# Performance work log

Hardware: AMD Instinct MI355X
Metric: run time of the kernel (lower is better)

The kernel has to match this reference:

```python
import jax, jax.numpy as jnp
import numpy as np

T, B, D, R, H = 16, 1024, 1024, 8, 16
DH = D // H


def setup_inputs() -> dict:
    key = jax.random.key(0)
    ks = jax.random.split(key, 10)
    s = 1.0 / np.sqrt(D)
    return {
        "table_embs": jax.random.normal(ks[0], (T, B, D), jnp.float32),
        "rel_embs": jax.random.normal(ks[1], (T, R, D), jnp.float32),
        "rel_idx": jax.random.randint(ks[2], (T, R), 0, T),
        "Wq": jax.random.normal(ks[3], (D, D), jnp.float32) * s,
        "bq": jnp.zeros((D,), jnp.float32),
        "Wk": jax.random.normal(ks[4], (D, D), jnp.float32) * s,
        "bk": jnp.zeros((D,), jnp.float32),
        "Wv": jax.random.normal(ks[5], (D, D), jnp.float32) * s,
        "bv": jnp.zeros((D,), jnp.float32),
        "Wo": jax.random.normal(ks[6], (D, D), jnp.float32) * s,
        "bo": jnp.zeros((D,), jnp.float32),
        "w_rel": jax.random.normal(ks[7], (D,), jnp.float32) * s,
        "b_rel": jnp.zeros((1,), jnp.float32),
    }


def reference(table_embs, rel_embs, rel_idx, Wq, bq, Wk, bk, Wv, bv, Wo, bo, w_rel, b_rel):
    # relationship weights: sigmoid(Linear(rel_emb)) -> scalar per (table, relation)
    rel_w = jax.nn.sigmoid(rel_embs @ w_rel + b_rel[0])          # [T, R]
    # gather related tables' embeddings and apply relationship weight
    others = table_embs[rel_idx]                                  # [T, R, B, D]
    weighted = others * rel_w[:, :, None, None]                   # [T, R, B, D]
    kv_src = jnp.transpose(weighted, (0, 2, 1, 3))                # [T, B, R, D]
    # MultiheadAttention, q_len=1, kv_len=R (PyTorch convention: x @ W.T + b)
    q = (table_embs @ Wq.T + bq).reshape(T, B, H, DH)             # [T, B, H, DH]
    k = (kv_src @ Wk.T + bk).reshape(T, B, R, H, DH)              # [T, B, R, H, DH]
    v = (kv_src @ Wv.T + bv).reshape(T, B, R, H, DH)
    scores = jnp.einsum("tbhd,tbrhd->tbhr", q, k) / np.sqrt(DH)   # [T, B, H, R]
    attn = jax.nn.softmax(scores, axis=-1)
    ctx = jnp.einsum("tbhr,tbrhd->tbhd", attn, v).reshape(T, B, D)
    return ctx @ Wo.T + bo                                        # [T, B, D]
```

## Files before the change

### kernel.cpp

```cpp
#include <hip/hip_runtime.h>


typedef unsigned short u16;
typedef __attribute__((ext_vector_type(8))) short short8;
typedef __attribute__((ext_vector_type(4))) float f32x4;

__device__ __forceinline__ float bf2f(u16 u) {
  unsigned int x = ((unsigned int)u) << 16;
  return __uint_as_float(x);
}
__device__ __forceinline__ u16 f2bf(float f) {
  unsigned int x = __float_as_uint(f);
  unsigned int r = (x + 0x7fffu + ((x >> 16) & 1u)) >> 16;
  return (u16)r;
}

__device__ __forceinline__ void gld_lds16(const void* g, void* l) {
  __builtin_amdgcn_global_load_lds(
      (const __attribute__((address_space(1))) unsigned int*)(unsigned long long)g,
      (__attribute__((address_space(3))) unsigned int*)(unsigned int)(unsigned long long)l,
      16, 0, 0);
}


__global__ void relw_kernel(const float* __restrict__ rel_embs,
                            const float* __restrict__ w_rel,
                            const float* __restrict__ b_rel,
                            float* __restrict__ rel_w) {
  const int tr = blockIdx.x;
  const float* row = rel_embs + (size_t)tr * 1024;
  const int lane = threadIdx.x;
  float s = 0.f;
  for (int i = lane; i < 1024; i += 64) s += row[i] * w_rel[i];
  for (int off = 32; off > 0; off >>= 1) s += __shfl_down(s, off, 64);
  if (lane == 0) rel_w[tr] = 1.f / (1.f + __expf(-(s + b_rel[0])));
}

__global__ void cvt_f32_bf16(const float* __restrict__ in, u16* __restrict__ out, int n4) {
  int i = blockIdx.x * blockDim.x + threadIdx.x;
  if (i >= n4) return;
  float4 v = ((const float4*)in)[i];
  ushort4 o;
  o.x = f2bf(v.x); o.y = f2bf(v.y); o.z = f2bf(v.z); o.w = f2bf(v.w);
  ((ushort4*)out)[i] = o;
}

__global__ void cvt_w4(const float* __restrict__ Wq, const float* __restrict__ Wk,
                       const float* __restrict__ Wv, const float* __restrict__ Wo,
                       u16* __restrict__ Wcat, u16* __restrict__ Wob) {
  const int i = blockIdx.x * 256 + threadIdx.x;
  const int w = i >> 18;
  const int j = i & 0x3ffff;
  const float* src = (w == 0) ? Wq : (w == 1) ? Wk : (w == 2) ? Wv : Wo;
  u16* dst = (w == 3) ? Wob : (Wcat + ((size_t)w << 20));
  float4 v = ((const float4*)src)[j];
  ushort4 o;
  o.x = f2bf(v.x); o.y = f2bf(v.y); o.z = f2bf(v.z); o.w = f2bf(v.w);
  ((ushort4*)dst)[j] = o;
}


__device__ __forceinline__ void mainloop256(const u16* __restrict__ A,
                                            const u16* __restrict__ B,
                                            u16* lds, int m0, int n0,
                                            f32x4 (&acc)[8][4]) {
  const int tid  = threadIdx.x;
  const int lane = tid & 63;
  const int w    = tid >> 6;
  const int wm   = w >> 2, wn = w & 3;
  const int fr   = lane & 15, fq = lane >> 4;
  const int swz  = fr & 7;

  const unsigned A0 = 0, B0 = 16384, A1 = 32768, B1 = 49152;

  const int srow = tid >> 3;
  const int lc   = (tid & 7) ^ (srow & 7);
  const u16* a0p = A + (size_t)(m0 + srow) * 1024 + lc * 8;
  const u16* b0p = B + (size_t)(n0 + srow) * 1024 + lc * 8;
  const unsigned d0 = (unsigned)((tid & ~63) * 8);

  const u16 *ap0[2], *ap1[2], *bp0[2], *bp1[2];
#pragma unroll
  for (int ks = 0; ks < 2; ++ks) {
    const unsigned ck = (unsigned)((((ks << 2) + fq) ^ swz) << 3);
    ap0[ks] = lds + A0 + (wm * 128 + fr) * 64 + ck;
    ap1[ks] = lds + A1 + (wm * 128 + fr) * 64 + ck;
    bp0[ks] = lds + B0 + (wn * 64 + fr) * 64 + ck;
    bp1[ks] = lds + B1 + (wn * 64 + fr) * 64 + ck;
  }

#define STAGE4(g, AO, BO)                                                      \
  do {                                                                         \
    gld_lds16(a0p + (2*(g))   * 65536, lds + (AO) + d0 + (2*(g))   * 4096);    \
    gld_lds16(a0p + (2*(g)+1) * 65536, lds + (AO) + d0 + (2*(g)+1) * 4096);    \
    gld_lds16(b0p + (2*(g))   * 65536, lds + (BO) + d0 + (2*(g))   * 4096);    \
    gld_lds16(b0p + (2*(g)+1) * 65536, lds + (BO) + d0 + (2*(g)+1) * 4096);    \
  } while (0)

#define PHASE_Q(q, ap, STMT)                                                   \
  do {                                                                         \
    short8 a0k0 = *(const short8*)((ap)[0] + (2*(q))   * 1024);                \
    short8 a1k0 = *(const short8*)((ap)[0] + (2*(q)+1) * 1024);                \
    short8 a0k1 = *(const short8*)((ap)[1] + (2*(q))   * 1024);                \
    short8 a1k1 = *(const short8*)((ap)[1] + (2*(q)+1) * 1024);                \
    STMT;                                                                      \
    __builtin_amdgcn_s_barrier();                                              \
    asm volatile("s_waitcnt lgkmcnt(0)" ::: "memory");                         \
    __builtin_amdgcn_sched_barrier(0);                                         \
    __builtin_amdgcn_s_setprio(1);                                             \
    _Pragma("unroll")                                                          \
    for (int j = 0; j < 4; ++j) {                                              \
      acc[2*(q)][j]   = __builtin_amdgcn_mfma_f32_16x16x32_bf16(a0k0, bgv[j][0], acc[2*(q)][j],   0, 0, 0); \
      acc[2*(q)+1][j] = __builtin_amdgcn_mfma_f32_16x16x32_bf16(a1k0, bgv[j][0], acc[2*(q)+1][j], 0, 0, 0); \
    }                                                                          \
    _Pragma("unroll")                                                          \
    for (int j = 0; j < 4; ++j) {                                              \
      acc[2*(q)][j]   = __builtin_amdgcn_mfma_f32_16x16x32_bf16(a0k1, bgv[j][1], acc[2*(q)][j],   0, 0, 0); \
      acc[2*(q)+1][j] = __builtin_amdgcn_mfma_f32_16x16x32_bf16(a1k1, bgv[j][1], acc[2*(q)+1][j], 0, 0, 0); \
    }                                                                          \
    __builtin_amdgcn_s_setprio(0);                                             \
  } while (0)

#define KTILE(ap, bp, AO_N, BO_N, SG)                                          \
  do {                                                                         \
    short8 bgv[4][2];                                                          \
    _Pragma("unroll")                                                          \
    for (int j = 0; j < 4; ++j) {                                              \
      bgv[j][0] = *(const short8*)((bp)[0] + j * 1024);                        \
      bgv[j][1] = *(const short8*)((bp)[1] + j * 1024);                        \
    }                                                                          \
    PHASE_Q(0, ap, { if (SG) STAGE4(0, AO_N, BO_N); });                        \
    __builtin_amdgcn_s_barrier();                                              \
    PHASE_Q(1, ap, { if (SG) { STAGE4(1, AO_N, BO_N); a0p += 64; b0p += 64; } }); \
    __builtin_amdgcn_s_barrier();                                              \
    PHASE_Q(2, ap, {});                                                        \
    __builtin_amdgcn_s_barrier();                                              \
    PHASE_Q(3, ap, {});                                                        \
    if (SG) asm volatile("s_waitcnt vmcnt(0)" ::: "memory");                   \
    __builtin_amdgcn_s_barrier();                                              \
  } while (0)

#pragma unroll
  for (int r = 0; r < 4; ++r) {
    gld_lds16(a0p + r * 65536, lds + A0 + d0 + r * 4096);
    gld_lds16(b0p + r * 65536, lds + B0 + d0 + r * 4096);
  }
  a0p += 64; b0p += 64;
  asm volatile("s_waitcnt vmcnt(0)" ::: "memory");
  __builtin_amdgcn_s_barrier();

  for (int it = 0; it < 8; ++it) {
    KTILE(ap0, bp0, A1, B1, true);
    KTILE(ap1, bp1, A0, B0, (it < 7));
  }
#undef STAGE4
#undef PHASE_Q
#undef KTILE
}

__global__ __launch_bounds__(512, 2)
void gemm_qkv(const u16* __restrict__ A, const u16* __restrict__ Bw,
              const float* __restrict__ bq,
              u16* __restrict__ Qt, u16* __restrict__ Kt, u16* __restrict__ Vt) {
  __shared__ __align__(16) u16 lds[65536];
  const int n0 = blockIdx.x * 256;
  const int m0 = blockIdx.y * 256;
  f32x4 acc[8][4];
#pragma unroll
  for (int i = 0; i < 8; ++i)
#pragma unroll
    for (int j = 0; j < 4; ++j) acc[i][j] = (f32x4){0.f, 0.f, 0.f, 0.f};

  mainloop256(A, Bw, lds, m0, n0, acc);

  const int tid  = threadIdx.x;
  const int lane = tid & 63;
  const int w    = tid >> 6;
  const int wm   = w >> 2, wn = w & 3;
  const int colw = lane & 15, roww = (lane >> 4) * 4;
  const int t = m0 >> 10, b0 = m0 & 1023;
  const int sel = n0 >> 10, dbase = n0 & 1023;
  u16* outp = (sel == 0) ? Qt : (sel == 1) ? Kt : Vt;

  for (int pass = 0; pass < 2; ++pass) {
    if (wm == pass) {
#pragma unroll
      for (int j = 0; j < 4; ++j) {
        const int dl = wn * 64 + j * 16 + colw;
        const float badd = (sel == 0) ? bq[dbase + dl] : 0.f;
#pragma unroll
        for (int i = 0; i < 8; ++i) {
          const int bl = i * 16 + roww;
          const unsigned p0 = (unsigned)f2bf(acc[i][j][0] + badd)
                            | ((unsigned)f2bf(acc[i][j][1] + badd) << 16);
          const unsigned p1 = (unsigned)f2bf(acc[i][j][2] + badd)
                            | ((unsigned)f2bf(acc[i][j][3] + badd) << 16);
          *(unsigned*)(lds + dl * 136 + bl)     = p0;
          *(unsigned*)(lds + dl * 136 + bl + 2) = p1;
        }
      }
    }
    __syncthreads();
#pragma unroll
    for (int rr = 0; rr < 8; ++rr) {
      const int slot = rr * 512 + tid;
      const int row = slot >> 4, c16 = slot & 15;
      const uint4 v = *(const uint4*)(lds + row * 136 + c16 * 8);
      *(uint4*)(outp + ((size_t)t << 20) + (size_t)(dbase + row) * 1024
                + b0 + pass * 128 + c16 * 8) = v;
    }
    __syncthreads();
  }
}

__global__ __launch_bounds__(512, 2)
void gemm_out(const u16* __restrict__ A, const u16* __restrict__ Bw,
              const float* __restrict__ bo, float* __restrict__ out) {
  __shared__ __align__(16) u16 lds[65536];
  const int n0 = blockIdx.x * 256;
  const int m0 = blockIdx.y * 256;
  f32x4 acc[8][4];
#pragma unroll
  for (int i = 0; i < 8; ++i)
#pragma unroll
    for (int j = 0; j < 4; ++j) acc[i][j] = (f32x4){0.f, 0.f, 0.f, 0.f};

  mainloop256(A, Bw, lds, m0, n0, acc);

  const int lane = threadIdx.x & 63;
  const int w    = threadIdx.x >> 6;
  const int wm   = w >> 2, wn = w & 3;
  const int colw = lane & 15, roww = (lane >> 4) * 4;
#pragma unroll
  for (int j = 0; j < 4; ++j) {
    const int gn = n0 + wn * 64 + j * 16 + colw;
    const float bov = bo[gn];
#pragma unroll
    for (int i = 0; i < 8; ++i) {
      const int gm = m0 + wm * 128 + i * 16 + roww;
#pragma unroll
      for (int r = 0; r < 4; ++r)
        out[(size_t)(gm + r) * 1024 + gn] = acc[i][j][r] + bov;
    }
  }
}

__global__ __launch_bounds__(256)
void attn5(const u16* __restrict__ Qt, const u16* __restrict__ Kt,
           const u16* __restrict__ Vt,
           const float* __restrict__ relw, const int* __restrict__ rel_idx,
           const float* __restrict__ bk, const float* __restrict__ bv,
           u16* __restrict__ ctx) {
  const int tid = threadIdx.x;
  const int h = blockIdx.y, t = blockIdx.z;
  const int b0 = blockIdx.x * 256;
  const int b = b0 + tid;
  const int hd = h * 64;

  __shared__ u16  st[256 * 34];
  __shared__ float bks[64], bvs[64], rws[8];
  __shared__ int   rids[8];

  if (tid < 64) { bks[tid] = bk[hd + tid]; bvs[tid] = bv[hd + tid]; }
  else if (tid < 72) { rws[tid - 64] = relw[t * 8 + (tid - 64)];
                       rids[tid - 64] = rel_idx[t * 8 + (tid - 64)]; }
  __syncthreads();

  const unsigned qoff = ((unsigned)t << 20) + ((unsigned)hd << 10) + (unsigned)b;
  unsigned koff[8];
#pragma unroll
  for (int r = 0; r < 8; ++r)
    koff[r] = ((unsigned)rids[r] << 20) + ((unsigned)hd << 10) + (unsigned)b;

  float acc[8];
#pragma unroll
  for (int r = 0; r < 8; ++r) acc[r] = 0.f;
  float qbk = 0.f;
#pragma unroll 4
  for (int d = 0; d < 64; ++d) {
    const float q = bf2f(Qt[qoff + d * 1024]);
    qbk += q * bks[d];
#pragma unroll
    for (int r = 0; r < 8; ++r)
      acc[r] += q * bf2f(Kt[koff[r] + d * 1024]);
  }

  float w[8];
  {
    float s[8], mx = -1e30f;
#pragma unroll
    for (int r = 0; r < 8; ++r) {
      s[r] = (rws[r] * acc[r] + qbk) * 0.125f;
      mx = fmaxf(mx, s[r]);
    }
    float sum = 0.f;
#pragma unroll
    for (int r = 0; r < 8; ++r) { s[r] = __expf(s[r] - mx); sum += s[r]; }
    const float inv = 1.f / sum;
#pragma unroll
    for (int r = 0; r < 8; ++r) w[r] = s[r] * inv * rws[r];
  }

  for (int half = 0; half < 2; ++half) {
#pragma unroll
    for (int dp = 0; dp < 32; dp += 2) {
      const int d = half * 32 + dp;
      float o0 = bvs[d];
      float o1 = bvs[d + 1];
#pragma unroll
      for (int r = 0; r < 8; ++r) {
        o0 += w[r] * bf2f(Vt[koff[r] + d * 1024]);
        o1 += w[r] * bf2f(Vt[koff[r] + (d + 1) * 1024]);
      }
      const unsigned p = (unsigned)f2bf(o0) | ((unsigned)f2bf(o1) << 16);
      *(unsigned*)(st + tid * 34 + dp) = p;
    }
    __syncthreads();
    {
      const int sub = tid & 7;
      const int rbase = tid >> 3;
#pragma unroll
      for (int p = 0; p < 8; ++p) {
        const int row = p * 32 + rbase;
        const uint2 v = *(const uint2*)(st + row * 34 + sub * 4);
        *(uint2*)(ctx + ((size_t)(t * 1024 + b0 + row)) * 1024
                  + hd + half * 32 + sub * 4) = v;
      }
    }
    __syncthreads();
  }
}


extern "C" void kernel_launch(void* const* d_in, const int* in_sizes, int n_in,
                              void* d_out, int out_size, void* d_ws, size_t ws_size,
                              hipStream_t stream) {
  const float* table = (const float*)d_in[0];
  const float* rele  = (const float*)d_in[1];
  const int*   ridx  = (const int*)d_in[2];
  const float* Wq    = (const float*)d_in[3];
  const float* bq    = (const float*)d_in[4];
  const float* Wk    = (const float*)d_in[5];
  const float* bk    = (const float*)d_in[6];
  const float* Wv    = (const float*)d_in[7];
  const float* bv    = (const float*)d_in[8];
  const float* Wo    = (const float*)d_in[9];
  const float* bo    = (const float*)d_in[10];
  const float* wr    = (const float*)d_in[11];
  const float* br    = (const float*)d_in[12];
  float* out = (float*)d_out;

  char* ws = (char*)d_ws;
  const size_t MB = 1024 * 1024;
  u16*  Xbf  = (u16*)(ws);
  u16*  Kt   = (u16*)(ws + 32  * MB);
  u16*  Vt   = (u16*)(ws + 64  * MB);
  u16*  Qt   = (u16*)(ws + 96  * MB);
  u16*  Wcat = (u16*)(ws + 128 * MB);
  u16*  Wob  = (u16*)(ws + 134 * MB);
  float* relw = (float*)(ws + 136 * MB);
  u16*  ctxb = Xbf;

  relw_kernel<<<128, 64, 0, stream>>>(rele, wr, br, relw);
  cvt_f32_bf16<<<16384, 256, 0, stream>>>(table, Xbf, 4194304);
  cvt_w4<<<4096, 256, 0, stream>>>(Wq, Wk, Wv, Wo, Wcat, Wob);

  gemm_qkv<<<dim3(12, 64), 512, 0, stream>>>(Xbf, Wcat, bq, Qt, Kt, Vt);
  attn5<<<dim3(4, 16, 16), 256, 0, stream>>>(Qt, Kt, Vt, relw, ridx, bk, bv, ctxb);
  gemm_out<<<dim3(4, 64), 512, 0, stream>>>(ctxb, Wob, bo, out);
}
```

Measured before the change: 371.5 us.

## Split GEMM prefetch into B-then-A stages with partial vmcnt waits and XCD swizzle

Reworks the double-buffered GEMM mainloop so the next tile's B slice is issued in phase 0 and the A rows in phases 1 and 2. It replaces the full vmcnt(0) drain with partial waits (vmcnt 6 and 2), so compute on the current tile can overlap more of the outstanding global-to-LDS loads. The last iteration is peeled into a separate tile routine with no prefetch. Both GEMM kernels also remap block IDs so that neighbouring tiles land on the same XCD, aiming for better L2 reuse. The risk is that the partial-wait counts could allow LDS reads before the data arrives if they do not match the load order exactly.

```diff
diff --git a/kernel.cpp b/kernel.cpp
--- a/kernel.cpp
+++ b/kernel.cpp
@@ -21,6 +21,8 @@
       (__attribute__((address_space(3))) unsigned int*)(unsigned int)(unsigned long long)l,
       16, 0, 0);
 }
+
+#define VWAIT(N) asm volatile("s_waitcnt vmcnt(" #N ")" ::: "memory")
 
 
 __global__ void relw_kernel(const float* __restrict__ rel_embs,
@@ -89,12 +91,19 @@
     bp1[ks] = lds + B1 + (wn * 64 + fr) * 64 + ck;
   }
 
-#define STAGE4(g, AO, BO)                                                      \
+#define STAGE_B4(BO)                                                           \
   do {                                                                         \
-    gld_lds16(a0p + (2*(g))   * 65536, lds + (AO) + d0 + (2*(g))   * 4096);    \
-    gld_lds16(a0p + (2*(g)+1) * 65536, lds + (AO) + d0 + (2*(g)+1) * 4096);    \
-    gld_lds16(b0p + (2*(g))   * 65536, lds + (BO) + d0 + (2*(g))   * 4096);    \
-    gld_lds16(b0p + (2*(g)+1) * 65536, lds + (BO) + d0 + (2*(g)+1) * 4096);    \
+    gld_lds16(b0p + 0 * 65536, lds + (BO) + d0 + 0 * 4096);                    \
+    gld_lds16(b0p + 1 * 65536, lds + (BO) + d0 + 1 * 4096);                    \
+    gld_lds16(b0p + 2 * 65536, lds + (BO) + d0 + 2 * 4096);                    \
+    gld_lds16(b0p + 3 * 65536, lds + (BO) + d0 + 3 * 4096);                    \
+    b0p += 64;                                                                 \
+  } while (0)
+
+#define STAGE_A2(ra, rb, AO)                                                   \
+  do {                                                                         \
+    gld_lds16(a0p + (ra) * 65536, lds + (AO) + d0 + (ra) * 4096);              \
+    gld_lds16(a0p + (rb) * 65536, lds + (AO) + d0 + (rb) * 4096);              \
   } while (0)
 
 #define PHASE_Q(q, ap, STMT)                                                   \
@@ -121,41 +130,77 @@
     __builtin_amdgcn_s_setprio(0);                                             \
   } while (0)
 
-#define KTILE(ap, bp, AO_N, BO_N, SG)                                          \
+#define BGV_LOAD(bp)                                                           \
+  _Pragma("unroll")                                                            \
+  for (int j = 0; j < 4; ++j) {                                                \
+    bgv[j][0] = *(const short8*)((bp)[0] + j * 1024);                          \
+    bgv[j][1] = *(const short8*)((bp)[1] + j * 1024);                          \
+  }
+
+#define KTILE(ap, bp, AO_N, BO_N)                                              \
   do {                                                                         \
     short8 bgv[4][2];                                                          \
-    _Pragma("unroll")                                                          \
-    for (int j = 0; j < 4; ++j) {                                              \
-      bgv[j][0] = *(const short8*)((bp)[0] + j * 1024);                        \
-      bgv[j][1] = *(const short8*)((bp)[1] + j * 1024);                        \
-    }                                                                          \
-    PHASE_Q(0, ap, { if (SG) STAGE4(0, AO_N, BO_N); });                        \
-    __builtin_amdgcn_s_barrier();                                              \
-    PHASE_Q(1, ap, { if (SG) { STAGE4(1, AO_N, BO_N); a0p += 64; b0p += 64; } }); \
-    __builtin_amdgcn_s_barrier();                                              \
-    PHASE_Q(2, ap, {});                                                        \
-    __builtin_amdgcn_s_barrier();                                              \
-    PHASE_Q(3, ap, {});                                                        \
-    if (SG) asm volatile("s_waitcnt vmcnt(0)" ::: "memory");                   \
+    BGV_LOAD(bp);                                                              \
+    PHASE_Q(0, ap, { STAGE_B4(BO_N); });                                       \
+    __builtin_amdgcn_s_barrier();                                              \
+    PHASE_Q(1, ap, { STAGE_A2(0, 2, AO_N); });                                 \
+    VWAIT(6);                                                                  \
+    __builtin_amdgcn_s_barrier();                                              \
+    PHASE_Q(2, ap, { STAGE_A2(1, 3, AO_N); a0p += 64; });                      \
+    __builtin_amdgcn_s_barrier();                                              \
+    PHASE_Q(3, ap, {});                                                       \
+    VWAIT(2);                                                                  \
     __builtin_amdgcn_s_barrier();                                              \
   } while (0)
 
-#pragma unroll
-  for (int r = 0; r < 4; ++r) {
-    gld_lds16(a0p + r * 65536, lds + A0 + d0 + r * 4096);
-    gld_lds16(b0p + r * 65536, lds + B0 + d0 + r * 4096);
-  }
+#define KTILE_LAST(ap, bp)                                                     \
+  do {                                                                         \
+    short8 bgv[4][2];                                                          \
+    BGV_LOAD(bp);                                                              \
+    PHASE_Q(0, ap, {});                                                       \
+    __builtin_amdgcn_s_barrier();                                              \
+    PHASE_Q(1, ap, {});                                                       \
+    VWAIT(0);                                                                  \
+    __builtin_amdgcn_s_barrier();                                              \
+    PHASE_Q(2, ap, {});                                                       \
+    __builtin_amdgcn_s_barrier();                                              \
+    PHASE_Q(3, ap, {});                                                       \
+    __builtin_amdgcn_s_barrier();                                              \
+  } while (0)
+
+  gld_lds16(b0p + 0 * 65536, lds + B0 + d0 + 0 * 4096);
+  gld_lds16(b0p + 1 * 65536, lds + B0 + d0 + 1 * 4096);
+  gld_lds16(b0p + 2 * 65536, lds + B0 + d0 + 2 * 4096);
+  gld_lds16(b0p + 3 * 65536, lds + B0 + d0 + 3 * 4096);
+  gld_lds16(a0p + 0 * 65536, lds + A0 + d0 + 0 * 4096);
+  gld_lds16(a0p + 2 * 65536, lds + A0 + d0 + 2 * 4096);
+  gld_lds16(a0p + 1 * 65536, lds + A0 + d0 + 1 * 4096);
+  gld_lds16(a0p + 3 * 65536, lds + A0 + d0 + 3 * 4096);
   a0p += 64; b0p += 64;
-  asm volatile("s_waitcnt vmcnt(0)" ::: "memory");
+  VWAIT(2);
   __builtin_amdgcn_s_barrier();
 
-  for (int it = 0; it < 8; ++it) {
-    KTILE(ap0, bp0, A1, B1, true);
-    KTILE(ap1, bp1, A0, B0, (it < 7));
-  }
-#undef STAGE4
+  for (int it = 0; it < 7; ++it) {
+    KTILE(ap0, bp0, A1, B1);
+    KTILE(ap1, bp1, A0, B0);
+  }
+  KTILE(ap0, bp0, A1, B1);
+  KTILE_LAST(ap1, bp1);
+
+#undef STAGE_B4
+#undef STAGE_A2
 #undef PHASE_Q
+#undef BGV_LOAD
 #undef KTILE
+#undef KTILE_LAST
+}
+
+__device__ __forceinline__ void xcd_swizzle(int nx, int ny, int& bx, int& by) {
+  const int nwg = nx * ny;
+  int bid = by * nx + bx;
+  bid = (bid & 7) * (nwg >> 3) + (bid >> 3);
+  bx = bid % nx;
+  by = bid / nx;
 }
 
 __global__ __launch_bounds__(512, 2)
@@ -163,8 +208,10 @@
               const float* __restrict__ bq,
               u16* __restrict__ Qt, u16* __restrict__ Kt, u16* __restrict__ Vt) {
   __shared__ __align__(16) u16 lds[65536];
-  const int n0 = blockIdx.x * 256;
-  const int m0 = blockIdx.y * 256;
+  int bx = blockIdx.x, by = blockIdx.y;
+  xcd_swizzle(gridDim.x, gridDim.y, bx, by);
+  const int n0 = bx * 256;
+  const int m0 = by * 256;
   f32x4 acc[8][4];
 #pragma unroll
   for (int i = 0; i < 8; ++i)
@@ -217,8 +264,10 @@
 void gemm_out(const u16* __restrict__ A, const u16* __restrict__ Bw,
               const float* __restrict__ bo, float* __restrict__ out) {
   __shared__ __align__(16) u16 lds[65536];
-  const int n0 = blockIdx.x * 256;
-  const int m0 = blockIdx.y * 256;
+  int bx = blockIdx.x, by = blockIdx.y;
+  xcd_swizzle(gridDim.x, gridDim.y, bx, by);
+  const int n0 = bx * 256;
+  const int m0 = by * 256;
   f32x4 acc[8][4];
 #pragma unroll
   for (int i = 0; i < 8; ++i)
```

New measurement: 365.8 us. Within noise of the previous version (-1.5%).
